# Performance work log

Hardware: AMD Instinct MI355X
Metric: run time of the kernel (lower is better)

## Reference

```python
import jax, jax.numpy as jnp
import numpy as np

N_NODES = 100000
N_EDGES = 1000000
N_INPUT = 64
N_HIDDEN = 64
K = 8


def setup_inputs() -> dict:
    key = jax.random.key(0)
    k1, k2, k3, k4 = jax.random.split(key, 4)
    x = jax.random.normal(k1, (N_NODES, N_INPUT), dtype=jnp.float32)
    edge_index = jax.random.randint(k2, (2, N_EDGES), 0, N_NODES, dtype=jnp.int64)
    # ChebConv has K independent [in, out] weight matrices (Glorot-ish scale) and a bias.
    weight = jax.random.normal(k3, (K, N_INPUT, N_HIDDEN), dtype=jnp.float32) * (1.0 / np.sqrt(N_INPUT))
    bias = jax.random.normal(k4, (N_HIDDEN,), dtype=jnp.float32) * 0.01
    return {"x": x, "edge_index": edge_index, "weight": weight, "bias": bias}


def _cheb_edge_norm(edge_index, num_nodes):
    # PyG ChebConv sym normalization with default lambda_max=2.0:
    #   L_hat = (2/lambda_max) * (I - D^-1/2 A D^-1/2) - I = -D^-1/2 A D^-1/2
    # (the diagonal +1 from the Laplacian and the -1 self-loop cancel exactly).
    src, dst = edge_index[0], edge_index[1]
    ones = jnp.ones(src.shape[0], dtype=jnp.float32)
    deg = jax.ops.segment_sum(ones, src, num_segments=num_nodes)
    deg_inv_sqrt = jnp.where(deg > 0, jax.lax.rsqrt(jnp.maximum(deg, 1.0)), 0.0)
    return -deg_inv_sqrt[src] * deg_inv_sqrt[dst]  # [E]


def reference(x, edge_index, weight, bias):
    num_nodes = x.shape[0]
    src, dst = edge_index[0], edge_index[1]
    norm = _cheb_edge_norm(edge_index, num_nodes)

    def prop(h):  # h: [N, F] -> L_hat @ h via gather-multiply-scatter over edges
        return jax.ops.segment_sum(norm[:, None] * h[src], dst, num_segments=num_nodes)

    # Chebyshev recursion: T0 = x, T1 = L_hat x, Tk = 2 L_hat T_{k-1} - T_{k-2}
    Tx0 = x
    out = Tx0 @ weight[0]
    Tx1 = prop(Tx0)
    out = out + Tx1 @ weight[1]
    for k in range(2, weight.shape[0]):
        Tx2 = 2.0 * prop(Tx1) - Tx0
        out = out + Tx2 @ weight[k]
        Tx0, Tx1 = Tx1, Tx2
    out = out + bias
    # bn=False path: ReLU then dropout (identity in eval mode)
    return jax.nn.relu(out)
```

## Files before the change

### kernel.cpp

```cpp
#include <hip/hip_runtime.h>
#include <hip/hip_bf16.h>

typedef __attribute__((ext_vector_type(8))) short s16x8;
typedef __attribute__((ext_vector_type(4))) float f32x4;

#define HC 48
#define RBH 16000
#define RBS 16000

static __device__ __forceinline__ unsigned short f2bf(float f) {
    unsigned int u = __float_as_uint(f);
    unsigned int r = (u + 0x7FFFu + ((u >> 16) & 1u)) >> 16;
    return (unsigned short)r;
}

__global__ __launch_bounds__(256) void k_hist(const int* __restrict__ eidx,
                                              unsigned short* __restrict__ partials,
                                              int N, int E, int HR) {
    __shared__ int h[RBH];
    int b = blockIdx.x;
    int job = b / (HR * HC);
    int rc = b % (HR * HC);
    int r = rc / HC, c = rc % HC;
    int lo = r * RBH;
    int nb = min(RBH, N - lo);
    if (nb <= 0) return;
    for (int i = threadIdx.x; i < nb; i += 256) h[i] = 0;
    __syncthreads();
    const int* vals = eidx + (size_t)job * E;
    int e0 = (int)(((long long)E * c / HC) & ~3LL);
    int e1 = (c == HC - 1) ? E : (int)(((long long)E * (c + 1) / HC) & ~3LL);
    int e = e0 + threadIdx.x * 4;
    for (; e + 4 <= e1; e += 1024) {
        int4 v = *reinterpret_cast<const int4*>(vals + e);
        unsigned r0 = (unsigned)(v.x - lo), r1 = (unsigned)(v.y - lo);
        unsigned r2 = (unsigned)(v.z - lo), r3 = (unsigned)(v.w - lo);
        if (r0 < (unsigned)nb) atomicAdd(&h[r0], 1);
        if (r1 < (unsigned)nb) atomicAdd(&h[r1], 1);
        if (r2 < (unsigned)nb) atomicAdd(&h[r2], 1);
        if (r3 < (unsigned)nb) atomicAdd(&h[r3], 1);
    }
    if (threadIdx.x == 0)
        for (int t = e1 & ~3; t < e1; ++t) {
            unsigned rel = (unsigned)(vals[t] - lo);
            if (rel < (unsigned)nb) atomicAdd(&h[rel], 1);
        }
    __syncthreads();
    unsigned short* outp = partials + ((size_t)(job * HC + c)) * N + lo;
    for (int i = threadIdx.x; i < nb; i += 256) outp[i] = (unsigned short)h[i];
}

__global__ void k_reduce(const unsigned short* __restrict__ partials,
                         float* __restrict__ dis, int* __restrict__ cnt, int N) {
    int n = blockIdx.x * blockDim.x + threadIdx.x;
    if (n >= N) return;
    int dsum = 0, csum = 0;
    for (int c = 0; c < HC; ++c) {
        dsum += partials[(size_t)c * N + n];
        csum += partials[(size_t)(HC + c) * N + n];
    }
    dis[n] = dsum > 0 ? rsqrtf((float)dsum) : 0.f;
    cnt[n] = csum;
}

__global__ void k_scan1(const int* __restrict__ cnt, int* __restrict__ incl,
                        int* __restrict__ bsum, int N) {
    __shared__ int sm[1024];
    int t = threadIdx.x;
    int i = blockIdx.x * 1024 + t;
    sm[t] = (i < N) ? cnt[i] : 0;
    __syncthreads();
    for (int off = 1; off < 1024; off <<= 1) {
        int add = (t >= off) ? sm[t - off] : 0;
        __syncthreads();
        sm[t] += add;
        __syncthreads();
    }
    if (i < N) incl[i] = sm[t];
    if (t == 1023) bsum[blockIdx.x] = sm[1023];
}

__global__ void k_scan2(const int* __restrict__ bsum, int* __restrict__ boff,
                        int nb, int* __restrict__ rowptr, int N) {
    if (threadIdx.x == 0 && blockIdx.x == 0) {
        int run = 0;
        for (int b = 0; b < nb; ++b) { boff[b] = run; run += bsum[b]; }
        rowptr[N] = run;
    }
}

__global__ void k_scan3(const int* __restrict__ cnt, const int* __restrict__ boff,
                        int* __restrict__ rowptr,
                        const unsigned short* __restrict__ pdst,
                        int* __restrict__ cbase, int N) {
    int i = blockIdx.x * 1024 + threadIdx.x;
    if (i >= N) return;
    int ex = rowptr[i] - cnt[i] + boff[blockIdx.x];
    rowptr[i] = ex;
    int run = ex;
    for (int c = 0; c < HC; ++c) {
        size_t idx = (size_t)c * N + i;
        cbase[idx] = run;
        run += pdst[idx];
    }
}

__global__ __launch_bounds__(256) void k_scatter(
        const int* __restrict__ src, const int* __restrict__ dst,
        const int* __restrict__ cbase, int* __restrict__ srcs, int N, int E) {
    __shared__ int cur[RBS];
    int r = blockIdx.x / HC, c = blockIdx.x % HC;
    int lo = r * RBS;
    int nb = min(RBS, N - lo);
    if (nb <= 0) return;
    for (int i = threadIdx.x; i < nb; i += 256)
        cur[i] = cbase[(size_t)c * N + lo + i];
    __syncthreads();
    int e0 = (int)(((long long)E * c / HC) & ~3LL);
    int e1 = (c == HC - 1) ? E : (int)(((long long)E * (c + 1) / HC) & ~3LL);
    int e = e0 + threadIdx.x * 4;
    for (; e + 4 <= e1; e += 1024) {
        int4 d4 = *reinterpret_cast<const int4*>(dst + e);
        unsigned r0 = (unsigned)(d4.x - lo), r1 = (unsigned)(d4.y - lo);
        unsigned r2 = (unsigned)(d4.z - lo), r3 = (unsigned)(d4.w - lo);
        if (r0 < (unsigned)nb) srcs[atomicAdd(&cur[r0], 1)] = src[e];
        if (r1 < (unsigned)nb) srcs[atomicAdd(&cur[r1], 1)] = src[e + 1];
        if (r2 < (unsigned)nb) srcs[atomicAdd(&cur[r2], 1)] = src[e + 2];
        if (r3 < (unsigned)nb) srcs[atomicAdd(&cur[r3], 1)] = src[e + 3];
    }
    if (threadIdx.x == 0)
        for (int t = e1 & ~3; t < e1; ++t) {
            unsigned rel = (unsigned)(dst[t] - lo);
            if (rel < (unsigned)nb) srcs[atomicAdd(&cur[rel], 1)] = src[t];
        }
}

__global__ void k_pack(const float* __restrict__ x, const float* __restrict__ dis,
                       const float* __restrict__ W,
                       unsigned short* __restrict__ tb0, unsigned short* __restrict__ ysA,
                       unsigned short* __restrict__ ysB, unsigned short* __restrict__ wt,
                       int N, int K) {
    int t = blockIdx.x * blockDim.x + threadIdx.x;
    int nys = (N + 1) * 32;
    if (t < nys) {
        int row = t >> 5, p = t & 31;
        size_t o = ((size_t)row << 6) + (p << 1);
        if (row == N) {
            *(unsigned*)(ysA + o) = 0;
            *(unsigned*)(ysB + o) = 0;
            return;
        }
        float2 v = *reinterpret_cast<const float2*>(x + o);
        float dv = dis[row];
        *(unsigned*)(tb0 + o) = (unsigned)f2bf(v.x) | ((unsigned)f2bf(v.y) << 16);
        *(unsigned*)(ysA + o) = (unsigned)f2bf(v.x * dv) | ((unsigned)f2bf(v.y * dv) << 16);
    } else {
        int u = t - nys;
        if (u < K * 4096) {
            float v = W[u];
            int k = u >> 12;
            int r = u & 4095;
            int i = r >> 6;
            int j = r & 63;
            wt[(size_t)j * (K * 64) + (k << 6) + i] = f2bf(v);
        }
    }
}

static __device__ __forceinline__ void addrow(float* acc, uint4 t) {
    acc[0] += __uint_as_float(t.x << 16);
    acc[1] += __uint_as_float(t.x & 0xffff0000u);
    acc[2] += __uint_as_float(t.y << 16);
    acc[3] += __uint_as_float(t.y & 0xffff0000u);
    acc[4] += __uint_as_float(t.z << 16);
    acc[5] += __uint_as_float(t.z & 0xffff0000u);
    acc[6] += __uint_as_float(t.w << 16);
    acc[7] += __uint_as_float(t.w & 0xffff0000u);
}

__global__ __launch_bounds__(256) void k_prop(
        const unsigned short* __restrict__ Ysin,
        const unsigned short* __restrict__ Tm2,
        unsigned short* __restrict__ Tout,
        unsigned short* __restrict__ Ysout,
        const int* __restrict__ rowptr, const int* __restrict__ srcs,
        const float* __restrict__ dis,
        int N, int E, float scale, float beta, int wys) {
    int gt = blockIdx.x * blockDim.x + threadIdx.x;
    int wave0 = (gt >> 6) << 3;
    int lane = gt & 63;
    int g = lane >> 3;
    int i = lane & 7;
    int node = wave0 + g;
    bool live = node < N;
    int rs = 0, deg = 0;
    if (live) {
        rs = rowptr[node];
        deg = rowptr[node + 1] - rs;
    }
    int wmax = deg;
#pragma unroll
    for (int m = 8; m <= 32; m <<= 1) {
        int o = __shfl_xor(wmax, m);
        wmax = o > wmax ? o : wmax;
    }
    float acc[8];
#pragma unroll
    for (int j = 0; j < 8; ++j) acc[j] = 0.f;
    for (int e = 0; e < wmax; e += 8) {
        int b = rs + e;
        int s[8];
#pragma unroll
        for (int q = 0; q < 8; ++q)
            s[q] = (e + q < deg) ? srcs[min(b + q, E - 1)] : N;
        uint4 t[8];
#pragma unroll
        for (int q = 0; q < 8; ++q)
            t[q] = *reinterpret_cast<const uint4*>(Ysin + ((size_t)s[q] << 6) + (i << 3));
#pragma unroll
        for (int q = 0; q < 8; ++q) addrow(acc, t[q]);
    }
    if (live) {
        float dv = dis[node];
        float sc = -scale * dv;
        size_t base = ((size_t)node << 6) + (i << 3);
        float r[8];
#pragma unroll
        for (int j = 0; j < 8; ++j) r[j] = sc * acc[j];
        if (beta != 0.f) {
            uint4 pv = *reinterpret_cast<const uint4*>(Tm2 + base);
            r[0] = fmaf(beta, __uint_as_float(pv.x << 16), r[0]);
            r[1] = fmaf(beta, __uint_as_float(pv.x & 0xffff0000u), r[1]);
            r[2] = fmaf(beta, __uint_as_float(pv.y << 16), r[2]);
            r[3] = fmaf(beta, __uint_as_float(pv.y & 0xffff0000u), r[3]);
            r[4] = fmaf(beta, __uint_as_float(pv.z << 16), r[4]);
            r[5] = fmaf(beta, __uint_as_float(pv.z & 0xffff0000u), r[5]);
            r[6] = fmaf(beta, __uint_as_float(pv.w << 16), r[6]);
            r[7] = fmaf(beta, __uint_as_float(pv.w & 0xffff0000u), r[7]);
        }
        uint4 ov;
        ov.x = (unsigned)f2bf(r[0]) | ((unsigned)f2bf(r[1]) << 16);
        ov.y = (unsigned)f2bf(r[2]) | ((unsigned)f2bf(r[3]) << 16);
        ov.z = (unsigned)f2bf(r[4]) | ((unsigned)f2bf(r[5]) << 16);
        ov.w = (unsigned)f2bf(r[6]) | ((unsigned)f2bf(r[7]) << 16);
        *reinterpret_cast<uint4*>(Tout + base) = ov;
        if (wys) {
            uint4 yv;
            yv.x = (unsigned)f2bf(r[0] * dv) | ((unsigned)f2bf(r[1] * dv) << 16);
            yv.y = (unsigned)f2bf(r[2] * dv) | ((unsigned)f2bf(r[3] * dv) << 16);
            yv.z = (unsigned)f2bf(r[4] * dv) | ((unsigned)f2bf(r[5] * dv) << 16);
            yv.w = (unsigned)f2bf(r[6] * dv) | ((unsigned)f2bf(r[7] * dv) << 16);
            *reinterpret_cast<uint4*>(Ysout + base) = yv;
        }
    }
}

template <int KS>
__global__ __launch_bounds__(256) void k_gemm(const unsigned short* __restrict__ tb,
                                              const unsigned short* __restrict__ wt,
                                              const float* __restrict__ bias,
                                              float* __restrict__ out,
                                              int N, int NF) {
    constexpr int NB = KS / 2;
    __shared__ unsigned short lds[KS * 512];
    int lane = threadIdx.x & 63;
    int w = threadIdx.x >> 6;
    int l16 = lane & 15;
    int quad = lane >> 4;
    const int KI = KS * 32;

    s16x8 afr[KS];
    {
        const unsigned short* wrow = wt + (size_t)(w * 16 + l16) * KI + quad * 8;
#pragma unroll
        for (int ks = 0; ks < KS; ++ks)
            afr[ks] = *reinterpret_cast<const s16x8*>(wrow + ks * 32);
    }
    f32x4 bias4 = *reinterpret_cast<const f32x4*>(bias + w * 16 + quad * 4);

    int ntiles = N >> 4;
    for (int t = blockIdx.x; t < ntiles; t += gridDim.x) {
        const char* tilebase = (const char*)tb + (size_t)t * 2048;
#pragma unroll
        for (int inst = 0; inst < 2 * NB; ++inst) {
            if ((inst & 3) != w) continue;
            int kbuf = inst >> 1;
            int j = inst & 1;
            int p = j * 64 + lane;
            int nrow = p >> 3;
            int s = (p & 7) ^ (nrow & 7);
            const char* g = tilebase + (size_t)kbuf * NF * 2 + nrow * 128 + s * 16;
            __builtin_amdgcn_global_load_lds(
                (const __attribute__((address_space(1))) unsigned int*)g,
                (__attribute__((address_space(3))) unsigned int*)(lds + inst * 512),
                16, 0, 0);
        }
        __syncthreads();
        f32x4 acc = {0.f, 0.f, 0.f, 0.f};
#pragma unroll
        for (int ks = 0; ks < KS; ++ks) {
            int kbuf = ks >> 1, half = ks & 1;
            int sph = (half * 4 + quad) ^ (l16 & 7);
            s16x8 bf = *reinterpret_cast<const s16x8*>(
                lds + kbuf * 1024 + l16 * 64 + sph * 8);
            acc = __builtin_amdgcn_mfma_f32_16x16x32_bf16(afr[ks], bf, acc, 0, 0, 0);
        }
        float* orow = out + (size_t)(t * 16 + l16) * 64 + w * 16 + quad * 4;
        f32x4 r;
#pragma unroll
        for (int q = 0; q < 4; ++q) {
            float v = acc[q] + bias4[q];
            r[q] = v > 0.f ? v : 0.f;
        }
        *reinterpret_cast<f32x4*>(orow) = r;
        __syncthreads();
    }
}

extern "C" void kernel_launch(void* const* d_in, const int* in_sizes, int n_in,
                              void* d_out, int out_size, void* d_ws, size_t ws_size,
                              hipStream_t stream) {
    const float* x    = (const float*)d_in[0];
    const int*   eidx = (const int*)d_in[1];
    const float* W    = (const float*)d_in[2];
    const float* bias = (const float*)d_in[3];
    float* out = (float*)d_out;

    const int NF = in_sizes[0];
    const int N  = NF / 64;
    const int E  = in_sizes[1] / 2;
    const int K  = in_sizes[2] / 4096;

    const int* src = eidx;
    const int* dst = eidx + E;

    char* ws = (char*)d_ws;
    size_t off = 0;
    auto alloc = [&](size_t bytes) -> char* {
        char* p = ws + off;
        off = (off + bytes + 255) & ~(size_t)255;
        return p;
    };
    unsigned short* Tb = (unsigned short*)alloc((size_t)K * NF * 2);
    unsigned short* Ys[2];
    Ys[0] = (unsigned short*)alloc((size_t)(N + 1) * 64 * 2);
    Ys[1] = (unsigned short*)alloc((size_t)(N + 1) * 64 * 2);
    unsigned short* Wt = (unsigned short*)alloc((size_t)64 * K * 64 * 2);
    int*   srcs   = (int*)alloc((size_t)E * 4);
    int*   rowptr = (int*)alloc((size_t)(N + 1) * 4);
    int*   cnt    = (int*)alloc((size_t)N * 4);
    unsigned short* partials = (unsigned short*)alloc((size_t)2 * HC * N * 2);
    int*   cbase  = (int*)alloc((size_t)HC * N * 4);
    float* dis  = (float*)alloc((size_t)N * 4);
    int*   bsum = (int*)alloc(1024);
    int*   boff = (int*)alloc(1024);
    (void)ws_size; (void)n_in; (void)out_size;

    int HR = (N + RBH - 1) / RBH;
    int SR = (N + RBS - 1) / RBS;
    const unsigned short* pdst = partials + (size_t)HC * N;

    k_hist<<<2 * HR * HC, 256, 0, stream>>>(eidx, partials, N, E, HR);
    k_reduce<<<(N + 255) / 256, 256, 0, stream>>>(partials, dis, cnt, N);
    int nb = (N + 1023) / 1024;
    k_scan1<<<nb, 1024, 0, stream>>>(cnt, rowptr, bsum, N);
    k_scan2<<<1, 64, 0, stream>>>(bsum, boff, nb, rowptr, N);
    k_scan3<<<nb, 1024, 0, stream>>>(cnt, boff, rowptr, pdst, cbase, N);
    k_scatter<<<SR * HC, 256, 0, stream>>>(src, dst, cbase, srcs, N, E);
    int packn = (N + 1) * 32 + K * 4096;
    k_pack<<<(packn + 255) / 256, 256, 0, stream>>>(x, dis, W, Tb, Ys[0], Ys[1], Wt, N, K);

    int waves = (N + 7) / 8;
    int pblocks = (waves * 64 + 255) / 256;
    for (int p = 1; p < K; ++p) {
        float scale = (p == 1) ? 1.f : 2.f;
        float beta  = (p == 1) ? 0.f : -1.f;
        const unsigned short* Tm2 = Tb + (size_t)(p >= 2 ? p - 2 : 0) * NF;
        k_prop<<<pblocks, 256, 0, stream>>>(
            Ys[(p - 1) & 1], Tm2, Tb + (size_t)p * NF, Ys[p & 1],
            rowptr, srcs, dis, N, E, scale, beta, p < K - 1 ? 1 : 0);
    }

    if (K == 8)      k_gemm<16><<<1024, 256, 0, stream>>>(Tb, Wt, bias, out, N, NF);
    else if (K == 4) k_gemm<8><<<1024, 256, 0, stream>>>(Tb, Wt, bias, out, N, NF);
    else if (K == 2) k_gemm<4><<<1024, 256, 0, stream>>>(Tb, Wt, bias, out, N, NF);
    else if (K == 1) k_gemm<2><<<1024, 256, 0, stream>>>(Tb, Wt, bias, out, N, NF);
}
```

Measured before the change: 348.2 us.

## Replace partitioned LDS histogram CSR build with global atomics and fused scans

Replaces the chunked shared-memory histogram, partial reduction, three-kernel scan and partitioned scatter with global-atomic degree counting, a fused rsqrt+block scan, a single-pass offset finalization, and a global-atomic scatter. This removes the large partials/cbase buffers and several launches, cutting memory traffic and launch overhead in CSR construction. In exchange it relies on global atomics (contention on hot nodes) and makes the within-row edge order nondeterministic, which can change floating-point summation order. The k_fin block-sum scan assumes at most 128 blocks.

```diff
diff --git a/kernel.cpp b/kernel.cpp
--- a/kernel.cpp
+++ b/kernel.cpp
@@ -3,10 +3,6 @@
 
 typedef __attribute__((ext_vector_type(8))) short s16x8;
 typedef __attribute__((ext_vector_type(4))) float f32x4;
-
-#define HC 48
-#define RBH 16000
-#define RBS 16000
 
 static __device__ __forceinline__ unsigned short f2bf(float f) {
     unsigned int u = __float_as_uint(f);
@@ -14,61 +10,41 @@
     return (unsigned short)r;
 }
 
-__global__ __launch_bounds__(256) void k_hist(const int* __restrict__ eidx,
-                                              unsigned short* __restrict__ partials,
-                                              int N, int E, int HR) {
-    __shared__ int h[RBH];
-    int b = blockIdx.x;
-    int job = b / (HR * HC);
-    int rc = b % (HR * HC);
-    int r = rc / HC, c = rc % HC;
-    int lo = r * RBH;
-    int nb = min(RBH, N - lo);
-    if (nb <= 0) return;
-    for (int i = threadIdx.x; i < nb; i += 256) h[i] = 0;
-    __syncthreads();
-    const int* vals = eidx + (size_t)job * E;
-    int e0 = (int)(((long long)E * c / HC) & ~3LL);
-    int e1 = (c == HC - 1) ? E : (int)(((long long)E * (c + 1) / HC) & ~3LL);
-    int e = e0 + threadIdx.x * 4;
-    for (; e + 4 <= e1; e += 1024) {
-        int4 v = *reinterpret_cast<const int4*>(vals + e);
-        unsigned r0 = (unsigned)(v.x - lo), r1 = (unsigned)(v.y - lo);
-        unsigned r2 = (unsigned)(v.z - lo), r3 = (unsigned)(v.w - lo);
-        if (r0 < (unsigned)nb) atomicAdd(&h[r0], 1);
-        if (r1 < (unsigned)nb) atomicAdd(&h[r1], 1);
-        if (r2 < (unsigned)nb) atomicAdd(&h[r2], 1);
-        if (r3 < (unsigned)nb) atomicAdd(&h[r3], 1);
-    }
-    if (threadIdx.x == 0)
-        for (int t = e1 & ~3; t < e1; ++t) {
-            unsigned rel = (unsigned)(vals[t] - lo);
-            if (rel < (unsigned)nb) atomicAdd(&h[rel], 1);
-        }
-    __syncthreads();
-    unsigned short* outp = partials + ((size_t)(job * HC + c)) * N + lo;
-    for (int i = threadIdx.x; i < nb; i += 256) outp[i] = (unsigned short)h[i];
-}
-
-__global__ void k_reduce(const unsigned short* __restrict__ partials,
-                         float* __restrict__ dis, int* __restrict__ cnt, int N) {
-    int n = blockIdx.x * blockDim.x + threadIdx.x;
-    if (n >= N) return;
-    int dsum = 0, csum = 0;
-    for (int c = 0; c < HC; ++c) {
-        dsum += partials[(size_t)c * N + n];
-        csum += partials[(size_t)(HC + c) * N + n];
-    }
-    dis[n] = dsum > 0 ? rsqrtf((float)dsum) : 0.f;
-    cnt[n] = csum;
-}
-
-__global__ void k_scan1(const int* __restrict__ cnt, int* __restrict__ incl,
-                        int* __restrict__ bsum, int N) {
+__global__ __launch_bounds__(256) void k_deg(const int* __restrict__ src,
+                                             const int* __restrict__ dst,
+                                             int* __restrict__ degS,
+                                             int* __restrict__ cnt, int E) {
+    int e = (blockIdx.x * 256 + threadIdx.x) * 4;
+    if (e + 4 <= E) {
+        int4 s4 = *reinterpret_cast<const int4*>(src + e);
+        int4 d4 = *reinterpret_cast<const int4*>(dst + e);
+        atomicAdd(&degS[s4.x], 1); atomicAdd(&degS[s4.y], 1);
+        atomicAdd(&degS[s4.z], 1); atomicAdd(&degS[s4.w], 1);
+        atomicAdd(&cnt[d4.x], 1);  atomicAdd(&cnt[d4.y], 1);
+        atomicAdd(&cnt[d4.z], 1);  atomicAdd(&cnt[d4.w], 1);
+    } else {
+        for (int t = e; t < E; ++t) {
+            atomicAdd(&degS[src[t]], 1);
+            atomicAdd(&cnt[dst[t]], 1);
+        }
+    }
+}
+
+__global__ __launch_bounds__(1024) void k_rs(const int* __restrict__ degS,
+                                             const int* __restrict__ cnt,
+                                             float* __restrict__ dis,
+                                             int* __restrict__ incl,
+                                             int* __restrict__ bsum, int N) {
     __shared__ int sm[1024];
     int t = threadIdx.x;
     int i = blockIdx.x * 1024 + t;
-    sm[t] = (i < N) ? cnt[i] : 0;
+    int csum = 0;
+    if (i < N) {
+        int d = degS[i];
+        dis[i] = d > 0 ? rsqrtf((float)d) : 0.f;
+        csum = cnt[i];
+    }
+    sm[t] = csum;
     __syncthreads();
     for (int off = 1; off < 1024; off <<= 1) {
         int add = (t >= off) ? sm[t - off] : 0;
@@ -80,59 +56,47 @@
     if (t == 1023) bsum[blockIdx.x] = sm[1023];
 }
 
-__global__ void k_scan2(const int* __restrict__ bsum, int* __restrict__ boff,
-                        int nb, int* __restrict__ rowptr, int N) {
-    if (threadIdx.x == 0 && blockIdx.x == 0) {
-        int run = 0;
-        for (int b = 0; b < nb; ++b) { boff[b] = run; run += bsum[b]; }
-        rowptr[N] = run;
-    }
-}
-
-__global__ void k_scan3(const int* __restrict__ cnt, const int* __restrict__ boff,
-                        int* __restrict__ rowptr,
-                        const unsigned short* __restrict__ pdst,
-                        int* __restrict__ cbase, int N) {
-    int i = blockIdx.x * 1024 + threadIdx.x;
+__global__ __launch_bounds__(1024) void k_fin(const int* __restrict__ cnt,
+                                              const int* __restrict__ bsum,
+                                              int* __restrict__ rowptr,
+                                              int* __restrict__ cur, int N, int nb) {
+    __shared__ int sb[128];
+    int t = threadIdx.x;
+    if (t < 128) sb[t] = (t < nb) ? bsum[t] : 0;
+    __syncthreads();
+    for (int off = 1; off < 128; off <<= 1) {
+        int add = (t < 128 && t >= off) ? sb[t - off] : 0;
+        __syncthreads();
+        if (t < 128) sb[t] += add;
+        __syncthreads();
+    }
+    int b = blockIdx.x;
+    int boff = (b == 0) ? 0 : sb[b - 1];
+    int total = sb[nb - 1];
+    int i = b * 1024 + t;
     if (i >= N) return;
-    int ex = rowptr[i] - cnt[i] + boff[blockIdx.x];
+    int ex = rowptr[i] - cnt[i] + boff;
     rowptr[i] = ex;
-    int run = ex;
-    for (int c = 0; c < HC; ++c) {
-        size_t idx = (size_t)c * N + i;
-        cbase[idx] = run;
-        run += pdst[idx];
-    }
-}
-
-__global__ __launch_bounds__(256) void k_scatter(
-        const int* __restrict__ src, const int* __restrict__ dst,
-        const int* __restrict__ cbase, int* __restrict__ srcs, int N, int E) {
-    __shared__ int cur[RBS];
-    int r = blockIdx.x / HC, c = blockIdx.x % HC;
-    int lo = r * RBS;
-    int nb = min(RBS, N - lo);
-    if (nb <= 0) return;
-    for (int i = threadIdx.x; i < nb; i += 256)
-        cur[i] = cbase[(size_t)c * N + lo + i];
-    __syncthreads();
-    int e0 = (int)(((long long)E * c / HC) & ~3LL);
-    int e1 = (c == HC - 1) ? E : (int)(((long long)E * (c + 1) / HC) & ~3LL);
-    int e = e0 + threadIdx.x * 4;
-    for (; e + 4 <= e1; e += 1024) {
+    cur[i] = ex;
+    if (i == N - 1) rowptr[N] = total;
+}
+
+__global__ __launch_bounds__(256) void k_scatter2(const int* __restrict__ src,
+                                                  const int* __restrict__ dst,
+                                                  int* __restrict__ cur,
+                                                  int* __restrict__ srcs, int E) {
+    int e = (blockIdx.x * 256 + threadIdx.x) * 4;
+    if (e + 4 <= E) {
+        int4 s4 = *reinterpret_cast<const int4*>(src + e);
         int4 d4 = *reinterpret_cast<const int4*>(dst + e);
-        unsigned r0 = (unsigned)(d4.x - lo), r1 = (unsigned)(d4.y - lo);
-        unsigned r2 = (unsigned)(d4.z - lo), r3 = (unsigned)(d4.w - lo);
-        if (r0 < (unsigned)nb) srcs[atomicAdd(&cur[r0], 1)] = src[e];
-        if (r1 < (unsigned)nb) srcs[atomicAdd(&cur[r1], 1)] = src[e + 1];
-        if (r2 < (unsigned)nb) srcs[atomicAdd(&cur[r2], 1)] = src[e + 2];
-        if (r3 < (unsigned)nb) srcs[atomicAdd(&cur[r3], 1)] = src[e + 3];
-    }
-    if (threadIdx.x == 0)
-        for (int t = e1 & ~3; t < e1; ++t) {
-            unsigned rel = (unsigned)(dst[t] - lo);
-            if (rel < (unsigned)nb) srcs[atomicAdd(&cur[rel], 1)] = src[t];
-        }
+        srcs[atomicAdd(&cur[d4.x], 1)] = s4.x;
+        srcs[atomicAdd(&cur[d4.y], 1)] = s4.y;
+        srcs[atomicAdd(&cur[d4.z], 1)] = s4.z;
+        srcs[atomicAdd(&cur[d4.w], 1)] = s4.w;
+    } else {
+        for (int t = e; t < E; ++t)
+            srcs[atomicAdd(&cur[dst[t]], 1)] = src[t];
+    }
 }
 
 __global__ void k_pack(const float* __restrict__ x, const float* __restrict__ dis,
@@ -349,24 +313,21 @@
     int*   srcs   = (int*)alloc((size_t)E * 4);
     int*   rowptr = (int*)alloc((size_t)(N + 1) * 4);
     int*   cnt    = (int*)alloc((size_t)N * 4);
-    unsigned short* partials = (unsigned short*)alloc((size_t)2 * HC * N * 2);
-    int*   cbase  = (int*)alloc((size_t)HC * N * 4);
+    int*   degS   = (int*)alloc((size_t)N * 4);
+    int*   cur    = (int*)alloc((size_t)N * 4);
     float* dis  = (float*)alloc((size_t)N * 4);
     int*   bsum = (int*)alloc(1024);
-    int*   boff = (int*)alloc(1024);
     (void)ws_size; (void)n_in; (void)out_size;
 
-    int HR = (N + RBH - 1) / RBH;
-    int SR = (N + RBS - 1) / RBS;
-    const unsigned short* pdst = partials + (size_t)HC * N;
-
-    k_hist<<<2 * HR * HC, 256, 0, stream>>>(eidx, partials, N, E, HR);
-    k_reduce<<<(N + 255) / 256, 256, 0, stream>>>(partials, dis, cnt, N);
+    hipMemsetAsync(cnt, 0, (size_t)N * 4, stream);
+    hipMemsetAsync(degS, 0, (size_t)N * 4, stream);
+
+    int eblocks = (E / 4 + 255) / 256 + 1;
+    k_deg<<<eblocks, 256, 0, stream>>>(src, dst, degS, cnt, E);
     int nb = (N + 1023) / 1024;
-    k_scan1<<<nb, 1024, 0, stream>>>(cnt, rowptr, bsum, N);
-    k_scan2<<<1, 64, 0, stream>>>(bsum, boff, nb, rowptr, N);
-    k_scan3<<<nb, 1024, 0, stream>>>(cnt, boff, rowptr, pdst, cbase, N);
-    k_scatter<<<SR * HC, 256, 0, stream>>>(src, dst, cbase, srcs, N, E);
+    k_rs<<<nb, 1024, 0, stream>>>(degS, cnt, dis, rowptr, bsum, N);
+    k_fin<<<nb, 1024, 0, stream>>>(cnt, bsum, rowptr, cur, N, nb);
+    k_scatter2<<<eblocks, 256, 0, stream>>>(src, dst, cur, srcs, E);
     int packn = (N + 1) * 32 + K * 4096;
     k_pack<<<(packn + 255) / 256, 256, 0, stream>>>(x, dis, W, Tb, Ys[0], Ys[1], Wt, N, K);
 
```

Measured after the change: 428.9 us. 23.2% more time.
